# Optimization experiments

Measured on AMD Instinct MI355X. Metric: run time of the kernel, lower is better.

Reference implementation:

```python
import jax, jax.numpy as jnp
import numpy as np

P = 9    # patch_size (number of shifts per axis)
DP = 1   # dilation_patch (pixel step per shift)


def setup_inputs() -> dict:
    key = jax.random.key(0)
    k1, k2 = jax.random.split(key)
    input1 = jax.random.normal(k1, (4, 256, 96, 128), dtype=jnp.float32)
    input2 = jax.random.normal(k2, (4, 256, 96, 128), dtype=jnp.float32)
    return {"input1": input1, "input2": input2}


def _correlation(input1, input2):
    # Faithful to iter_spatial_correlation_sample with kernel_size=1, stride=1,
    # padding=0, dilation=1: offsets are integer pixel shifts, and bilinear
    # grid_sample (align_corners=True, zeros outside) at integer coordinates is
    # exactly a zero-padded integer shift of input2.
    b, c, h, w = input2.shape
    off = DP * ((P - 1) // 2)  # center offset in pixels
    pad2 = jnp.pad(input2, ((0, 0), (0, 0), (off, off), (off, off)))
    rows = []
    for i in range(P):          # small fixed loop over patch offsets (81 total)
        cols = []
        for j in range(P):
            # window = input2 shifted by (dy, dx) = (i*DP - off, j*DP - off)
            win = jax.lax.dynamic_slice(pad2, (0, 0, i * DP, j * DP), (b, c, h, w))
            cols.append(jnp.einsum('bchw,bchw->bhw', input1, win))
        rows.append(jnp.stack(cols, axis=1))  # [b, P, h, w]
    return jnp.stack(rows, axis=1)            # [b, P, P, h, w]


def reference(input1, input2):
    return _correlation(input1, input2)
```

## Files before the change

kernel.cpp:

```cpp
#include <hip/hip_runtime.h>

#define CC 256
#define HH 96
#define WW 128
#define PP 9
#define OFF 4
#define PLANE (HH * WW)

#define HB 3
#define PX 32
#define SW 48
#define PAD 20
#define KCH 32
#define NCHK (CC / KCH)
#define TPB 384
#define RNMAX 7
#define DPAD 36
#define NU 4
#define ADVB (KCH * PLANE * 4)

typedef _Float16 f16x8 __attribute__((ext_vector_type(8)));
typedef float fx4 __attribute__((ext_vector_type(4)));

union U16 { uint4 u; f16x8 h; };

__device__ __forceinline__ unsigned pk(float a, float b) {
#if __has_builtin(__builtin_amdgcn_cvt_pkrtz)
  auto r = __builtin_amdgcn_cvt_pkrtz(a, b);
  unsigned u; __builtin_memcpy(&u, &r, 4); return u;
#else
  _Float16 h0 = (_Float16)a, h1 = (_Float16)b;
  unsigned u = 0, v = 0; __builtin_memcpy(&u, &h0, 2); __builtin_memcpy(&v, &h1, 2);
  return u | (v << 16);
#endif
}

__global__ __launch_bounds__(TPB, 5) void corr_kernel(const float* __restrict__ in1,
                                                      const float* __restrict__ in2,
                                                      float* __restrict__ out) {
  __shared__ __align__(16) unsigned s2[RNMAX][SW][PAD];
  __shared__ __align__(16) unsigned s1[HB][PX][PAD];

  const int bx = blockIdx.x;
  const int xcd = bx & 7;
  const int s = bx >> 3;
  const int half = s & 1;
  const int xq = (s >> 1) & 3;
  const int b = (s >> 3) & 3;
  const int bl = s >> 5;
  const int band = xcd * 4 + bl;
  const int h0 = band * HB;
  const int d0 = half ? 5 : 0;
  const int ndy = half ? 4 : 5;
  const int rnw = ndy + HB - 1;

  const int tid = threadIdx.x;
  const int wv = tid >> 6;
  const int wr = wv >> 1;
  const int wp = wv & 1;
  const int lane = tid & 63;
  const int ln = lane & 15;
  const int lg = lane >> 4;

  const char* in2p = (const char*)in2;
  const char* in1p = (const char*)in1;

  const int spx = tid % 48;
  const int sq = tid / 48;
  const int scb = sq & 3;
  const int sr0 = sq >> 2;
  const int gx2 = xq * PX - OFF + spx;
  const bool okx = (unsigned)gx2 < WW;

  unsigned o2[NU];
  unsigned vmask = 0;
#pragma unroll
  for (int k = 0; k < NU; ++k) {
    const int r = sr0 + 2 * k;
    const int rg = h0 - OFF + d0 + r;
    const bool ok = (r < rnw) && okx && ((unsigned)rg < HH);
    o2[k] = ok ? (unsigned)(((b * CC + scb * 8) * PLANE + rg * WW + gx2) * 4) : 0u;
    vmask |= (ok ? 1u : 0u) << k;
  }
  const int tpx = tid & 31;
  const int tq = tid >> 5;
  const int tcb = tq & 3;
  const int tr = tq >> 2;
  const unsigned o1 = (unsigned)(((b * CC + tcb * 8) * PLANE + (h0 + tr) * WW + xq * PX + tpx) * 4);

  for (int i = tid; i < RNMAX * SW * PAD; i += TPB) ((unsigned*)s2)[i] = 0u;

  fx4 acc[5][2];
#pragma unroll
  for (int d = 0; d < 5; ++d)
#pragma unroll
    for (int t = 0; t < 2; ++t) acc[d][t] = (fx4)0.f;

  __syncthreads();

#pragma unroll 1
  for (int c = 0; c < NCHK; ++c) {
    const unsigned cadv = (unsigned)c * ADVB;
#pragma unroll
    for (int k = 0; k < NU; ++k)
      if ((vmask >> k) & 1) {
        const float* p = (const float*)(in2p + (o2[k] + cadv));
        const float l0 = p[0], l1 = p[PLANE], l2 = p[2 * PLANE], l3 = p[3 * PLANE];
        const float l4 = p[4 * PLANE], l5 = p[5 * PLANE], l6 = p[6 * PLANE], l7 = p[7 * PLANE];
        uint4 w;
        w.x = pk(l0, l1); w.y = pk(l2, l3); w.z = pk(l4, l5); w.w = pk(l6, l7);
        *(uint4*)&s2[sr0 + 2 * k][spx][4 * scb] = w;
      }
    {
      const float* p = (const float*)(in1p + (o1 + cadv));
      const float l0 = p[0], l1 = p[PLANE], l2 = p[2 * PLANE], l3 = p[3 * PLANE];
      const float l4 = p[4 * PLANE], l5 = p[5 * PLANE], l6 = p[6 * PLANE], l7 = p[7 * PLANE];
      uint4 w;
      w.x = pk(l0, l1); w.y = pk(l2, l3); w.z = pk(l4, l5); w.w = pk(l6, l7);
      *(uint4*)&s1[tr][tpx][4 * tcb] = w;
    }
    __syncthreads();

    U16 a; a.u = *(const uint4*)&s1[wr][wp * 16 + ln][4 * lg];
#pragma unroll
    for (int d = 0; d < 5; ++d)
      if (d < ndy) {
#pragma unroll
        for (int t = 0; t < 2; ++t) {
          U16 bb; bb.u = *(const uint4*)&s2[wr + d][wp * 16 + 16 * t + ln][4 * lg];
          acc[d][t] = __builtin_amdgcn_mfma_f32_16x16x32_f16(a.h, bb.h, acc[d][t], 0, 0, 0);
        }
      }
    __syncthreads();
  }

  float* DL = (float*)&s2[0][0][0];
#pragma unroll
  for (int d = 0; d < 5; ++d)
    if (d < ndy) {
#pragma unroll
      for (int t = 0; t < 2; ++t) {
        const int p2 = wp * 16 + 16 * t + ln;
        *(fx4*)&DL[(wr * SW + p2) * DPAD + wp * 16 + 4 * lg] = acc[d][t];
      }
      __syncthreads();
#pragma unroll
      for (int k2 = 0; k2 < 3; ++k2) {
        const int id = tid + TPB * k2;
        if (id < HB * PP * PX) {
          const int px = id & 31;
          const int v = id >> 5;
          const int dx = v % PP;
          const int rr = v / PP;
          out[(size_t)((b * PP + d0 + d) * PP + dx) * PLANE + (size_t)(h0 + rr) * WW + xq * PX + px] =
              DL[(rr * SW + px + dx) * DPAD + px];
        }
      }
      __syncthreads();
    }
}

extern "C" void kernel_launch(void* const* d_in, const int* in_sizes, int n_in,
                              void* d_out, int out_size, void* d_ws, size_t ws_size,
                              hipStream_t stream) {
  const float* in1 = (const float*)d_in[0];
  const float* in2 = (const float*)d_in[1];
  float* out = (float*)d_out;
  corr_kernel<<<dim3(1024), dim3(TPB), 0, stream>>>(in1, in2, out);
}
```

Before: 157.8 us.

## Double-buffer LDS staging and ping-pong the epilogue writeout

Adds second shared-memory buffers for both inputs so loading and converting the next channel chunk overlaps MFMA compute on the current one, halving the barriers per chunk. The epilogue also alternates two scratch buffers so writing one dy slice overlaps reading out the previous one. LDS use doubles and launch bounds occupancy drops from 5 to 3 blocks per CU, which reduces latency hiding from concurrent blocks.

```diff
diff --git a/kernel.cpp b/kernel.cpp
--- a/kernel.cpp
+++ b/kernel.cpp
@@ -35,11 +35,13 @@
 #endif
 }
 
-__global__ __launch_bounds__(TPB, 5) void corr_kernel(const float* __restrict__ in1,
+__global__ __launch_bounds__(TPB, 3) void corr_kernel(const float* __restrict__ in1,
                                                       const float* __restrict__ in2,
                                                       float* __restrict__ out) {
-  __shared__ __align__(16) unsigned s2[RNMAX][SW][PAD];
-  __shared__ __align__(16) unsigned s1[HB][PX][PAD];
+  __shared__ __align__(16) unsigned s2a[RNMAX][SW][PAD];
+  __shared__ __align__(16) unsigned s1a[HB][PX][PAD];
+  __shared__ __align__(16) unsigned s2b[RNMAX][SW][PAD];
+  __shared__ __align__(16) unsigned s1b[HB][PX][PAD];
 
   const int bx = blockIdx.x;
   const int xcd = bx & 7;
@@ -88,7 +90,10 @@
   const int tr = tq >> 2;
   const unsigned o1 = (unsigned)(((b * CC + tcb * 8) * PLANE + (h0 + tr) * WW + xq * PX + tpx) * 4);
 
-  for (int i = tid; i < RNMAX * SW * PAD; i += TPB) ((unsigned*)s2)[i] = 0u;
+  for (int i = tid; i < RNMAX * SW * PAD; i += TPB) {
+    ((unsigned*)s2a)[i] = 0u;
+    ((unsigned*)s2b)[i] = 0u;
+  }
 
   fx4 acc[5][2];
 #pragma unroll
@@ -96,11 +101,8 @@
 #pragma unroll
     for (int t = 0; t < 2; ++t) acc[d][t] = (fx4)0.f;
 
-  __syncthreads();
-
-#pragma unroll 1
-  for (int c = 0; c < NCHK; ++c) {
-    const unsigned cadv = (unsigned)c * ADVB;
+  auto STAGE = [&](unsigned (&S2)[RNMAX][SW][PAD], unsigned (&S1)[HB][PX][PAD], int c) {
+    const unsigned cadv = (unsigned)c * (unsigned)ADVB;
 #pragma unroll
     for (int k = 0; k < NU; ++k)
       if ((vmask >> k) & 1) {
@@ -109,7 +111,7 @@
         const float l4 = p[4 * PLANE], l5 = p[5 * PLANE], l6 = p[6 * PLANE], l7 = p[7 * PLANE];
         uint4 w;
         w.x = pk(l0, l1); w.y = pk(l2, l3); w.z = pk(l4, l5); w.w = pk(l6, l7);
-        *(uint4*)&s2[sr0 + 2 * k][spx][4 * scb] = w;
+        *(uint4*)&S2[sr0 + 2 * k][spx][4 * scb] = w;
       }
     {
       const float* p = (const float*)(in1p + (o1 + cadv));
@@ -117,47 +119,77 @@
       const float l4 = p[4 * PLANE], l5 = p[5 * PLANE], l6 = p[6 * PLANE], l7 = p[7 * PLANE];
       uint4 w;
       w.x = pk(l0, l1); w.y = pk(l2, l3); w.z = pk(l4, l5); w.w = pk(l6, l7);
-      *(uint4*)&s1[tr][tpx][4 * tcb] = w;
+      *(uint4*)&S1[tr][tpx][4 * tcb] = w;
     }
-    __syncthreads();
-
-    U16 a; a.u = *(const uint4*)&s1[wr][wp * 16 + ln][4 * lg];
+  };
+
+  auto COMPUTE = [&](const unsigned (&S2)[RNMAX][SW][PAD], const unsigned (&S1)[HB][PX][PAD]) {
+    U16 a; a.u = *(const uint4*)&S1[wr][wp * 16 + ln][4 * lg];
 #pragma unroll
     for (int d = 0; d < 5; ++d)
       if (d < ndy) {
 #pragma unroll
         for (int t = 0; t < 2; ++t) {
-          U16 bb; bb.u = *(const uint4*)&s2[wr + d][wp * 16 + 16 * t + ln][4 * lg];
+          U16 bb; bb.u = *(const uint4*)&S2[wr + d][wp * 16 + 16 * t + ln][4 * lg];
           acc[d][t] = __builtin_amdgcn_mfma_f32_16x16x32_f16(a.h, bb.h, acc[d][t], 0, 0, 0);
         }
       }
+  };
+
+  __syncthreads();
+  STAGE(s2a, s1a, 0);
+  __syncthreads();
+
+#pragma unroll 1
+  for (int cc = 0; cc < NCHK / 2; ++cc) {
+    STAGE(s2b, s1b, 2 * cc + 1);
+    COMPUTE(s2a, s1a);
+    __syncthreads();
+    if (cc < NCHK / 2 - 1) STAGE(s2a, s1a, 2 * cc + 2);
+    COMPUTE(s2b, s1b);
     __syncthreads();
   }
 
-  float* DL = (float*)&s2[0][0][0];
-#pragma unroll
-  for (int d = 0; d < 5; ++d)
-    if (d < ndy) {
-#pragma unroll
-      for (int t = 0; t < 2; ++t) {
-        const int p2 = wp * 16 + 16 * t + ln;
-        *(fx4*)&DL[(wr * SW + p2) * DPAD + wp * 16 + 4 * lg] = acc[d][t];
+  auto WRITED = [&](float* DL, const fx4 (&ad)[2]) {
+#pragma unroll
+    for (int t = 0; t < 2; ++t) {
+      const int p2 = wp * 16 + 16 * t + ln;
+      *(fx4*)&DL[(wr * SW + p2) * DPAD + wp * 16 + 4 * lg] = ad[t];
+    }
+  };
+  auto READOUT = [&](const float* DL, int dyg) {
+#pragma unroll
+    for (int k2 = 0; k2 < 3; ++k2) {
+      const int id = tid + TPB * k2;
+      if (id < HB * PP * PX) {
+        const int px = id & 31;
+        const int v = id >> 5;
+        const int dx = v % PP;
+        const int rr = v / PP;
+        out[(size_t)((b * PP + dyg) * PP + dx) * PLANE + (size_t)(h0 + rr) * WW + xq * PX + px] =
+            DL[(rr * SW + px + dx) * DPAD + px];
       }
-      __syncthreads();
-#pragma unroll
-      for (int k2 = 0; k2 < 3; ++k2) {
-        const int id = tid + TPB * k2;
-        if (id < HB * PP * PX) {
-          const int px = id & 31;
-          const int v = id >> 5;
-          const int dx = v % PP;
-          const int rr = v / PP;
-          out[(size_t)((b * PP + d0 + d) * PP + dx) * PLANE + (size_t)(h0 + rr) * WW + xq * PX + px] =
-              DL[(rr * SW + px + dx) * DPAD + px];
-        }
-      }
-      __syncthreads();
     }
+  };
+
+  float* DLA = (float*)&s2a[0][0][0];
+  float* DLB = (float*)&s2b[0][0][0];
+
+  WRITED(DLA, acc[0]);
+  __syncthreads();
+  if (1 < ndy) WRITED(DLB, acc[1]);
+  READOUT(DLA, d0 + 0);
+  __syncthreads();
+  if (2 < ndy) WRITED(DLA, acc[2]);
+  if (1 < ndy) READOUT(DLB, d0 + 1);
+  __syncthreads();
+  if (3 < ndy) WRITED(DLB, acc[3]);
+  if (2 < ndy) READOUT(DLA, d0 + 2);
+  __syncthreads();
+  if (4 < ndy) WRITED(DLA, acc[4]);
+  if (3 < ndy) READOUT(DLB, d0 + 3);
+  __syncthreads();
+  if (4 < ndy) READOUT(DLA, d0 + 4);
 }
 
 extern "C" void kernel_launch(void* const* d_in, const int* in_sizes, int n_in,
```

Result: slower. 187.0 us (+18.5%).
